# Performance work log

Measured on AMD Instinct MI355X. Metric: run time of the kernel, lower is better.

Reference implementation:

```python
import jax, jax.numpy as jnp
import numpy as np

TOP_K = 2
LORA_SCALE = 32.0 / 16.0  # alpha / rank


def setup_inputs() -> dict:
    key = jax.random.key(0)
    ks = jax.random.split(key, 11)
    N, D, F, E, R = 1024, 2048, 5632, 8, 16
    s = lambda k, shape, fan: jax.random.normal(k, shape, jnp.float32) / np.sqrt(fan)
    return {
        "x": jax.random.normal(ks[0], (N, D), jnp.float32),
        "gate_w": s(ks[1], (E, D), D),
        "W1": s(ks[2], (F, D), D),
        "W3": s(ks[3], (F, D), D),
        "W2": s(ks[4], (D, F), F),
        "A1": s(ks[5], (E, R, D), D),
        "B1": s(ks[6], (F, R), R)[None].repeat(E, 0) * 0.0 + s(ks[6], (E, F, R), R),
        "A3": s(ks[7], (E, R, D), D),
        "B3": s(ks[8], (E, F, R), R),
        "A2": s(ks[9], (E, R, F), F),
        "B2": s(ks[10], (E, D, R), R),
    }


def reference(x, gate_w, W1, W3, W2, A1, B1, A3, B3, A2, B2):
    # --- router: softmax over experts, top-k, renormalized combine weights ---
    logits = x @ gate_w.T                                   # [N, E]
    probs = jax.nn.softmax(logits, axis=-1)
    topw, topi = jax.lax.top_k(probs, TOP_K)                # [N, K]
    topw = topw / jnp.sum(topw, axis=-1, keepdims=True)
    E = gate_w.shape[0]
    w = jnp.sum(jax.nn.one_hot(topi, E, dtype=x.dtype) * topw[..., None], axis=1)  # [N, E]

    # --- experts: shared base weights + per-expert LoRA (fused SwiGLU) ---
    base1 = x @ W1.T                                        # [N, F]
    base3 = x @ W3.T                                        # [N, F]
    l1 = jnp.einsum("nd,erd->ner", x, A1)                   # rank-R bottleneck
    l3 = jnp.einsum("nd,erd->ner", x, A3)
    h1 = base1[:, None, :] + LORA_SCALE * jnp.einsum("ner,efr->nef", l1, B1)  # [N, E, F]
    h3 = base3[:, None, :] + LORA_SCALE * jnp.einsum("ner,efr->nef", l3, B3)
    s = jax.nn.silu(h1) * h3                                # [N, E, F]

    # down-projection: shared W2 applied to the routed mixture, plus per-expert LoRA
    s_mix = jnp.einsum("ne,nef->nf", w, s)                  # [N, F]
    out = s_mix @ W2.T                                      # [N, D]
    l2 = jnp.einsum("nef,erf->ner", s, A2) * (w[:, :, None] * LORA_SCALE)
    out = out + jnp.einsum("ner,edr->nd", l2, B2)           # [N, D]
    return out, logits
```

## Files before the change

kernel.cpp:

```cpp
#include <hip/hip_runtime.h>

typedef unsigned int u32;
typedef unsigned short u16;

#define N_TOK 1024
#define D_DIM 2048
#define F_DIM 5632
#define E_NUM 8
#define R_DIM 16
#define LSCALE 2.0f
#define FT 256
#define NT (F_DIM / FT)
#define TC 8
#define BN13 11520

typedef __bf16 bf16x8 __attribute__((ext_vector_type(8)));
typedef float f32x4 __attribute__((ext_vector_type(4)));
typedef u16 u16x8 __attribute__((ext_vector_type(8)));

__device__ inline u16 f2bf(float f) {
    u32 u = __builtin_bit_cast(u32, f);
    u32 r = (u + 0x7fffu + ((u >> 16) & 1u)) >> 16;
    return (u16)r;
}
__device__ inline float bf2f(u16 h) {
    u32 u = ((u32)h) << 16;
    return __builtin_bit_cast(float, u);
}

__global__ __launch_bounds__(256) void cvt_all(const float* __restrict__ x,
                                               const float* __restrict__ W1,
                                               const float* __restrict__ W3,
                                               const float* __restrict__ A1,
                                               const float* __restrict__ A3,
                                               const float* __restrict__ W2,
                                               const float* __restrict__ B1,
                                               const float* __restrict__ B3,
                                               u16* __restrict__ xb,
                                               u16* __restrict__ w13,
                                               u16* __restrict__ w2b,
                                               u16* __restrict__ b1b,
                                               u16* __restrict__ b3b) {
    int i = blockIdx.x * 256 + threadIdx.x;
    const float* src;
    u16* dst;
    int off;
    if (i < 524288)       { src = x;  dst = xb;             off = i; }
    else if (i < 3407872) { src = W1; dst = w13;            off = i - 524288; }
    else if (i < 6291456) { src = W3; dst = w13 + 11534336; off = i - 3407872; }
    else if (i < 6356992) { src = A1; dst = w13 + 23068672; off = i - 6291456; }
    else if (i < 6422528) { src = A3; dst = w13 + 23330816; off = i - 6356992; }
    else if (i < 9306112) { src = W2; dst = w2b;            off = i - 6422528; }
    else if (i < 9486336) { src = B1; dst = b1b;            off = i - 9306112; }
    else                  { src = B3; dst = b3b;            off = i - 9486336; }
    float4 v = ((const float4*)src)[off];
    union { u16 h[4]; ushort4 u4; } o;
    o.h[0] = f2bf(v.x); o.h[1] = f2bf(v.y); o.h[2] = f2bf(v.z); o.h[3] = f2bf(v.w);
    ((ushort4*)dst)[off] = o.u4;
}

__global__ __launch_bounds__(256) void a2_transpose(const float* __restrict__ A2,
                                                    u16* __restrict__ A2t) {
    int e = blockIdx.y;
    int f = blockIdx.x * 256 + threadIdx.x;
    u16 row[16];
#pragma unroll
    for (int r = 0; r < 16; ++r)
        row[r] = f2bf(A2[((size_t)e * R_DIM + r) * F_DIM + f]);
    u16* dst = A2t + ((size_t)e * F_DIM + f) * 16;
#pragma unroll
    for (int q = 0; q < 2; ++q)
        ((ulonglong2*)dst)[q] = ((ulonglong2*)row)[q];
}

__global__ __launch_bounds__(256) void router_kernel(const float* __restrict__ x,
                                                     const float* __restrict__ gw,
                                                     float* __restrict__ logits,
                                                     int* __restrict__ ridx,
                                                     float* __restrict__ rw) {
    int n = blockIdx.x;
    int tid = threadIdx.x;
    float part[E_NUM];
#pragma unroll
    for (int e = 0; e < E_NUM; ++e) part[e] = 0.f;
    const float* xr = x + (size_t)n * D_DIM;
    for (int d = tid; d < D_DIM; d += 256) {
        float xv = xr[d];
#pragma unroll
        for (int e = 0; e < E_NUM; ++e) part[e] += xv * gw[e * D_DIM + d];
    }
    __shared__ float sh[E_NUM][256];
#pragma unroll
    for (int e = 0; e < E_NUM; ++e) sh[e][tid] = part[e];
    __syncthreads();
    for (int off = 128; off > 0; off >>= 1) {
        if (tid < off) {
#pragma unroll
            for (int e = 0; e < E_NUM; ++e) sh[e][tid] += sh[e][tid + off];
        }
        __syncthreads();
    }
    if (tid == 0) {
        float lg[E_NUM], p[E_NUM];
        float mx = -1e30f;
        for (int e = 0; e < E_NUM; ++e) {
            lg[e] = sh[e][0];
            logits[n * E_NUM + e] = lg[e];
            if (lg[e] > mx) mx = lg[e];
        }
        float s = 0.f;
        for (int e = 0; e < E_NUM; ++e) { p[e] = expf(lg[e] - mx); s += p[e]; }
        for (int e = 0; e < E_NUM; ++e) p[e] /= s;
        int i1 = 0;
        for (int e = 1; e < E_NUM; ++e) if (p[e] > p[i1]) i1 = e;
        int i2 = (i1 == 0) ? 1 : 0;
        for (int e = 0; e < E_NUM; ++e) if (e != i1 && p[e] > p[i2]) i2 = e;
        float t = p[i1] + p[i2];
        ridx[n * 2] = i1; ridx[n * 2 + 1] = i2;
        rw[n * 2] = p[i1] / t; rw[n * 2 + 1] = p[i2] / t;
    }
}

__global__ __launch_bounds__(64) void zero_counts(int* counts) {
    if (threadIdx.x < E_NUM) counts[threadIdx.x] = 0;
}
__global__ __launch_bounds__(256) void build_lists(const int* __restrict__ ridx,
                                                   int* __restrict__ counts,
                                                   u32* __restrict__ lists) {
    int n = blockIdx.x * 256 + threadIdx.x;
    if (n >= N_TOK) return;
#pragma unroll
    for (int k = 0; k < 2; ++k) {
        int e = ridx[n * 2 + k];
        int slot = atomicAdd(&counts[e], 1);
        lists[e * N_TOK + slot] = (u32)n | ((u32)k << 16);
    }
}

__global__ __launch_bounds__(512, 2) void gemm256(const u16* __restrict__ A,
                                                  const u16* __restrict__ B,
                                                  float* __restrict__ C,
                                                  int N, int K, int kslice,
                                                  int mode, int ntm, int ntn) {
    __shared__ __align__(16) u16 sA[2][256 * 64];
    __shared__ __align__(16) u16 sB[2][256 * 64];

    const int nb = gridDim.x;
    const int f = blockIdx.x;
    const int q = nb >> 3, r = nb & 7;
    const int xcd = f & 7, lo = f >> 3;
    const int wg = (xcd < r ? xcd * (q + 1) : r * (q + 1) + (xcd - r) * q) + lo;

    const int mt = wg % ntm;
    const int t2 = wg / ntm;
    const int nt = t2 % ntn;
    const int zt = t2 / ntn;

    const int bm0 = mt * 256;
    const int bn0 = nt * 256;
    const int kb = zt * kslice;

    const int tid = threadIdx.x;
    const int lane = tid & 63;
    const int wave = tid >> 6;
    const int quad = lane >> 4;
    const int l16 = lane & 15;
    const int wm = (wave >> 2) * 128;
    const int wn = (wave & 3) * 64;

    f32x4 zero = {0.f, 0.f, 0.f, 0.f};
    f32x4 acc[8][4];
#pragma unroll
    for (int i = 0; i < 8; ++i)
#pragma unroll
        for (int j = 0; j < 4; ++j) acc[i][j] = zero;

    auto stage = [&](int buf, int k0) {
#pragma unroll
        for (int i = 0; i < 4; ++i) {
            int c = i * 512 + tid;
            int rr = c >> 3;
            int c8 = (c & 7) << 3;
            const u16* ga = A + (size_t)(bm0 + rr) * K + k0 + c8;
            const u16* gb = B + (size_t)(bn0 + rr) * K + k0 + c8;
            __builtin_amdgcn_global_load_lds((const __attribute__((address_space(1))) u32*)ga,
                                             (__attribute__((address_space(3))) u32*)(&sA[buf][c * 8]),
                                             16, 0, 0);
            __builtin_amdgcn_global_load_lds((const __attribute__((address_space(1))) u32*)gb,
                                             (__attribute__((address_space(3))) u32*)(&sB[buf][c * 8]),
                                             16, 0, 0);
        }
    };

    const int nk = kslice >> 6;
    int cur = 0;
    stage(0, kb);
    __syncthreads();

    for (int kt = 0; kt < nk; ++kt) {
        if (kt + 1 < nk) stage(cur ^ 1, kb + (kt + 1) * 64);
#pragma unroll
        for (int ks = 0; ks < 2; ++ks) {
            bf16x8 af[8], bfv[4];
#pragma unroll
            for (int mi = 0; mi < 8; ++mi)
                af[mi] = *(const bf16x8*)(&sA[cur][(wm + mi * 16 + l16) * 64 + ks * 32 + quad * 8]);
#pragma unroll
            for (int ni = 0; ni < 4; ++ni)
                bfv[ni] = *(const bf16x8*)(&sB[cur][(wn + ni * 16 + l16) * 64 + ks * 32 + quad * 8]);
#pragma unroll
            for (int mi = 0; mi < 8; ++mi)
#pragma unroll
                for (int ni = 0; ni < 4; ++ni)
                    acc[mi][ni] = __builtin_amdgcn_mfma_f32_16x16x32_bf16(af[mi], bfv[ni],
                                                                          acc[mi][ni], 0, 0, 0);
        }
        __syncthreads();
        cur ^= 1;
    }

#pragma unroll
    for (int mi = 0; mi < 8; ++mi)
#pragma unroll
        for (int ni = 0; ni < 4; ++ni) {
            int col = bn0 + wn + ni * 16 + l16;
#pragma unroll
            for (int i = 0; i < 4; ++i) {
                int row = bm0 + wm + mi * 16 + quad * 4 + i;
                if (mode == 1) {
                    ((u16*)C)[(size_t)row * N + col] = f2bf(acc[mi][ni][i]);
                } else if (mode == 2) {
                    unsafeAtomicAdd(&C[(size_t)row * N + col], acc[mi][ni][i]);
                } else {
                    C[(size_t)row * N + col] = acc[mi][ni][i];
                }
            }
        }
}

__global__ __launch_bounds__(256) void act_v2b(const u16* __restrict__ base13,
                                               const u16* __restrict__ B1b,
                                               const u16* __restrict__ B3b,
                                               const u32* __restrict__ lists,
                                               const int* __restrict__ counts,
                                               const float* __restrict__ rw,
                                               u16* __restrict__ sbuf) {
    const int ft = blockIdx.x;
    const int e  = blockIdx.y;
    const int z  = blockIdx.z;
    const int tid = threadIdx.x;
    const int lane = tid & 63;
    const int wave = tid >> 6;
    const int f_lane = ft * FT + lane * 4;

    u16x8 w1c[8], w3c[8];
    {
        const u16* p1 = B1b + ((size_t)e * F_DIM + f_lane) * 16;
        const u16* p3 = B3b + ((size_t)e * F_DIM + f_lane) * 16;
#pragma unroll
        for (int c = 0; c < 8; ++c) {
            w1c[c] = *(const u16x8*)(p1 + c * 8);
            w3c[c] = *(const u16x8*)(p3 + c * 8);
        }
    }

    const int T = counts[e];
    for (int i = z * 4 + wave; i < T; i += TC * 4) {
        u32 ent = lists[e * N_TOK + i];
        int n = (int)(ent & 0xFFFFu);
        int k = (int)(ent >> 16);
        float wt = rw[n * 2 + k];

        float la1[16], la3[16];
        {
            const u16x8* pl1 = (const u16x8*)(base13 + (size_t)n * BN13 + 11264 + e * 16);
            const u16x8* pl3 = (const u16x8*)(base13 + (size_t)n * BN13 + 11392 + e * 16);
#pragma unroll
            for (int h = 0; h < 2; ++h) {
                u16x8 t1 = pl1[h], t3 = pl3[h];
#pragma unroll
                for (int qq = 0; qq < 8; ++qq) {
                    la1[h * 8 + qq] = LSCALE * bf2f(t1[qq]);
                    la3[h * 8 + qq] = LSCALE * bf2f(t3[qq]);
                }
            }
        }

        ushort4 b1u = *(const ushort4*)(base13 + (size_t)n * BN13 + f_lane);
        ushort4 b3u = *(const ushort4*)(base13 + (size_t)n * BN13 + 5632 + f_lane);
        const u16* b1p = (const u16*)&b1u;
        const u16* b3p = (const u16*)&b3u;

        u16 sv[4];
#pragma unroll
        for (int j = 0; j < 4; ++j) {
            float h1 = bf2f(b1p[j]);
            float h3 = bf2f(b3p[j]);
#pragma unroll
            for (int qq = 0; qq < 8; ++qq) {
                h1 += la1[qq] * bf2f(w1c[2 * j][qq]);
                h3 += la3[qq] * bf2f(w3c[2 * j][qq]);
            }
#pragma unroll
            for (int qq = 0; qq < 8; ++qq) {
                h1 += la1[8 + qq] * bf2f(w1c[2 * j + 1][qq]);
                h3 += la3[8 + qq] * bf2f(w3c[2 * j + 1][qq]);
            }
            float sg = h1 / (1.f + __expf(-h1));
            sv[j] = f2bf(wt * sg * h3);
        }
        *(ushort4*)(sbuf + ((size_t)k * N_TOK + n) * F_DIM + f_lane) = *(ushort4*)sv;
    }
}

__global__ __launch_bounds__(256) void combine_kernel(const u16* __restrict__ sbuf,
                                                      u16* __restrict__ smix) {
    size_t i = ((size_t)blockIdx.x * 256 + threadIdx.x) * 8;
    u16x8 a = *(const u16x8*)(sbuf + i);
    u16x8 b = *(const u16x8*)(sbuf + (size_t)N_TOK * F_DIM + i);
    u16x8 o;
#pragma unroll
    for (int q = 0; q < 8; ++q) o[q] = f2bf(bf2f(a[q]) + bf2f(b[q]));
    *(u16x8*)(smix + i) = o;
}

__global__ __launch_bounds__(256) void lora_down_v3(const u16* __restrict__ sbuf,
                                                    const u16* __restrict__ A2t,
                                                    const int* __restrict__ ridx,
                                                    const float* __restrict__ B2,
                                                    float* __restrict__ out) {
    const int n = blockIdx.x, tid = threadIdx.x;
    __shared__ float part[2][32][16];
    __shared__ float fin[2][16];
    __shared__ int se[2];
    if (tid < 2) se[tid] = ridx[n * 2 + tid];
    __syncthreads();

    {
        const int k = tid >> 7;
        const int tt = tid & 127;
        const int rq = tt & 3;
        const int fc = tt >> 2;
        const int e = se[k];
        const u16* srow = sbuf + ((size_t)k * N_TOK + n) * F_DIM + fc * 176;
        const u16* arow = A2t + ((size_t)e * F_DIM + fc * 176) * 16 + rq * 4;
        float acc0 = 0.f, acc1 = 0.f, acc2 = 0.f, acc3 = 0.f;
#pragma unroll 4
        for (int f = 0; f < 176; ++f) {
            float sv = bf2f(srow[f]);
            ushort4 wr = *(const ushort4*)(arow + (size_t)f * 16);
            acc0 += sv * bf2f(wr.x);
            acc1 += sv * bf2f(wr.y);
            acc2 += sv * bf2f(wr.z);
            acc3 += sv * bf2f(wr.w);
        }
        part[k][fc][rq * 4 + 0] = acc0;
        part[k][fc][rq * 4 + 1] = acc1;
        part[k][fc][rq * 4 + 2] = acc2;
        part[k][fc][rq * 4 + 3] = acc3;
    }
    __syncthreads();
    if (tid < 32) {
        int k = tid >> 4, r = tid & 15;
        float s = 0.f;
#pragma unroll
        for (int fc = 0; fc < 32; ++fc) s += part[k][fc][r];
        fin[k][r] = LSCALE * s;
    }
    __syncthreads();

    float a0[16], a1v[16];
#pragma unroll
    for (int r = 0; r < 16; ++r) { a0[r] = fin[0][r]; a1v[r] = fin[1][r]; }
    const float* B2a = B2 + (size_t)se[0] * D_DIM * R_DIM;
    const float* B2b = B2 + (size_t)se[1] * D_DIM * R_DIM;
    float* orow = out + (size_t)n * D_DIM;
    for (int d = tid; d < D_DIM; d += 256) {
        const float4* pa = (const float4*)(B2a + (size_t)d * 16);
        const float4* pb = (const float4*)(B2b + (size_t)d * 16);
        float acc = 0.f;
#pragma unroll
        for (int q = 0; q < 4; ++q) {
            float4 va = pa[q];
            acc += a0[q * 4] * va.x + a0[q * 4 + 1] * va.y +
                   a0[q * 4 + 2] * va.z + a0[q * 4 + 3] * va.w;
            float4 vb = pb[q];
            acc += a1v[q * 4] * vb.x + a1v[q * 4 + 1] * vb.y +
                   a1v[q * 4 + 2] * vb.z + a1v[q * 4 + 3] * vb.w;
        }
        orow[d] = acc;
    }
}

extern "C" void kernel_launch(void* const* d_in, const int* in_sizes, int n_in,
                              void* d_out, int out_size, void* d_ws, size_t ws_size,
                              hipStream_t stream) {
    const float* x  = (const float*)d_in[0];
    const float* gw = (const float*)d_in[1];
    const float* W1 = (const float*)d_in[2];
    const float* W3 = (const float*)d_in[3];
    const float* W2 = (const float*)d_in[4];
    const float* A1 = (const float*)d_in[5];
    const float* B1 = (const float*)d_in[6];
    const float* A3 = (const float*)d_in[7];
    const float* B3 = (const float*)d_in[8];
    const float* A2 = (const float*)d_in[9];
    const float* B2 = (const float*)d_in[10];
    float* out = (float*)d_out;
    float* logits = out + (size_t)N_TOK * D_DIM;

    char* ws = (char*)d_ws;
    size_t off = 0;
    auto alloc = [&](size_t bytes) { char* p = ws + off; off += (bytes + 255) & ~(size_t)255; return p; };
    u16*   xb    = (u16*)alloc((size_t)N_TOK * D_DIM * 2);
    u16*   W13b  = (u16*)alloc((size_t)BN13 * D_DIM * 2);
    u16*   W2b   = (u16*)alloc((size_t)D_DIM * F_DIM * 2);
    u16*   base13= (u16*)alloc((size_t)N_TOK * BN13 * 2);
    int*   ridx  = (int*)alloc((size_t)N_TOK * 2 * 4);
    float* rwt   = (float*)alloc((size_t)N_TOK * 2 * 4);
    u16*   B1b   = (u16*)alloc((size_t)E_NUM * F_DIM * R_DIM * 2);
    u16*   B3b   = (u16*)alloc((size_t)E_NUM * F_DIM * R_DIM * 2);
    u16*   A2t   = (u16*)alloc((size_t)E_NUM * F_DIM * R_DIM * 2);
    int*   counts= (int*)alloc(64);
    u32*   lists = (u32*)alloc((size_t)E_NUM * N_TOK * 4);
    u16*   sbuf  = (u16*)alloc((size_t)2 * N_TOK * F_DIM * 2);
    u16*   smixb = (u16*)alloc((size_t)N_TOK * F_DIM * 2);
    (void)ws_size; (void)in_sizes; (void)n_in; (void)out_size;

    cvt_all<<<37760, 256, 0, stream>>>(x, W1, W3, A1, A3, W2, B1, B3,
                                       xb, W13b, W2b, B1b, B3b);
    a2_transpose<<<dim3(F_DIM / 256, E_NUM), 256, 0, stream>>>(A2, A2t);

    router_kernel<<<N_TOK, 256, 0, stream>>>(x, gw, logits, ridx, rwt);
    zero_counts<<<1, 64, 0, stream>>>(counts);
    build_lists<<<N_TOK / 256, 256, 0, stream>>>(ridx, counts, lists);

    gemm256<<<180, 512, 0, stream>>>(xb, W13b, (float*)base13,
                                     BN13, D_DIM, D_DIM, 1, 4, 45);

    act_v2b<<<dim3(NT, E_NUM, TC), 256, 0, stream>>>(base13, B1b, B3b,
                                                     lists, counts, rwt, sbuf);

    combine_kernel<<<(N_TOK * F_DIM / 8) / 256, 256, 0, stream>>>(sbuf, smixb);

    lora_down_v3<<<N_TOK, 256, 0, stream>>>(sbuf, A2t, ridx, B2, out);

    gemm256<<<256, 512, 0, stream>>>(smixb, W2b, out,
                                     D_DIM, F_DIM, 704, 2, 4, 8);
}
```

Measured before the change: 464.5 us.

## Restructure gemm256 mainloop into quadrant-staged pipeline with swizzled LDS

```diff
diff --git a/kernel.cpp b/kernel.cpp
--- a/kernel.cpp
+++ b/kernel.cpp
@@ -27,6 +27,11 @@
     u32 u = ((u32)h) << 16;
     return __builtin_bit_cast(float, u);
 }
+
+#define LGKM0() do { asm volatile("s_waitcnt lgkmcnt(0)" ::: "memory"); \
+                     __builtin_amdgcn_sched_barrier(0); } while (0)
+#define VMC(n)  do { asm volatile("s_waitcnt vmcnt(" #n ")" ::: "memory"); \
+                     __builtin_amdgcn_sched_barrier(0); } while (0)
 
 __global__ __launch_bounds__(256) void cvt_all(const float* __restrict__ x,
                                                const float* __restrict__ W1,
@@ -142,14 +147,13 @@
                                                   float* __restrict__ C,
                                                   int N, int K, int kslice,
                                                   int mode, int ntm, int ntn) {
-    __shared__ __align__(16) u16 sA[2][256 * 64];
-    __shared__ __align__(16) u16 sB[2][256 * 64];
+    __shared__ __align__(16) u16 lds[2][2][2][256 * 32];
 
     const int nb = gridDim.x;
-    const int f = blockIdx.x;
-    const int q = nb >> 3, r = nb & 7;
-    const int xcd = f & 7, lo = f >> 3;
-    const int wg = (xcd < r ? xcd * (q + 1) : r * (q + 1) + (xcd - r) * q) + lo;
+    const int fb = blockIdx.x;
+    const int qq = nb >> 3, rr = nb & 7;
+    const int xcd = fb & 7, lo = fb >> 3;
+    const int wg = (xcd < rr ? xcd * (qq + 1) : rr * (qq + 1) + (xcd - rr) * qq) + lo;
 
     const int mt = wg % ntm;
     const int t2 = wg / ntm;
@@ -165,6 +169,7 @@
     const int wave = tid >> 6;
     const int quad = lane >> 4;
     const int l16 = lane & 15;
+    const int swz = (l16 & 8) << 1;
     const int wm = (wave >> 2) * 128;
     const int wn = (wave & 3) * 64;
 
@@ -175,48 +180,139 @@
 #pragma unroll
         for (int j = 0; j < 4; ++j) acc[i][j] = zero;
 
-    auto stage = [&](int buf, int k0) {
-#pragma unroll
-        for (int i = 0; i < 4; ++i) {
-            int c = i * 512 + tid;
-            int rr = c >> 3;
-            int c8 = (c & 7) << 3;
-            const u16* ga = A + (size_t)(bm0 + rr) * K + k0 + c8;
-            const u16* gb = B + (size_t)(bn0 + rr) * K + k0 + c8;
-            __builtin_amdgcn_global_load_lds((const __attribute__((address_space(1))) u32*)ga,
-                                             (__attribute__((address_space(3))) u32*)(&sA[buf][c * 8]),
+    auto stageHalf = [&](const u16* __restrict__ G, int mat, int buf, int h,
+                         int k0, int rowBase) {
+#pragma unroll
+        for (int j = 0; j < 2; ++j) {
+            int seg = wave * 2 + j;
+            int plane = seg >> 3;
+            int rb = seg & 7;
+            int r = h * 128 + rb * 16 + (lane >> 2);
+            int slot = lane & 3;
+            int gcol = k0 + plane * 32 + ((slot * 8) ^ ((r & 8) << 1));
+            const u16* gp = G + (size_t)(rowBase + r) * K + gcol;
+            u16* lp = &lds[mat][buf][plane][(h * 128 + rb * 16) * 32] + lane * 8;
+            __builtin_amdgcn_global_load_lds((const __attribute__((address_space(1))) u32*)gp,
+                                             (__attribute__((address_space(3))) u32*)lp,
                                              16, 0, 0);
-            __builtin_amdgcn_global_load_lds((const __attribute__((address_space(1))) u32*)gb,
-                                             (__attribute__((address_space(3))) u32*)(&sB[buf][c * 8]),
-                                             16, 0, 0);
         }
     };
 
     const int nk = kslice >> 6;
-    int cur = 0;
-    stage(0, kb);
-    __syncthreads();
-
-    for (int kt = 0; kt < nk; ++kt) {
-        if (kt + 1 < nk) stage(cur ^ 1, kb + (kt + 1) * 64);
-#pragma unroll
-        for (int ks = 0; ks < 2; ++ks) {
-            bf16x8 af[8], bfv[4];
-#pragma unroll
-            for (int mi = 0; mi < 8; ++mi)
-                af[mi] = *(const bf16x8*)(&sA[cur][(wm + mi * 16 + l16) * 64 + ks * 32 + quad * 8]);
-#pragma unroll
-            for (int ni = 0; ni < 4; ++ni)
-                bfv[ni] = *(const bf16x8*)(&sB[cur][(wn + ni * 16 + l16) * 64 + ks * 32 + quad * 8]);
-#pragma unroll
-            for (int mi = 0; mi < 8; ++mi)
-#pragma unroll
-                for (int ni = 0; ni < 4; ++ni)
-                    acc[mi][ni] = __builtin_amdgcn_mfma_f32_16x16x32_bf16(af[mi], bfv[ni],
-                                                                          acc[mi][ni], 0, 0, 0);
-        }
-        __syncthreads();
-        cur ^= 1;
+
+    stageHalf(A, 0, 0, 0, kb, bm0);
+    stageHalf(A, 0, 0, 1, kb, bm0);
+    stageHalf(B, 1, 0, 0, kb, bn0);
+    stageHalf(B, 1, 0, 1, kb, bn0);
+    stageHalf(A, 0, 1, 0, kb + 64, bm0);
+    stageHalf(A, 0, 1, 1, kb + 64, bm0);
+    VMC(4);
+    __builtin_amdgcn_s_barrier();
+
+    bf16x8 af[8][2];
+    for (int t = 0; t < nk; ++t) {
+        const int buf = t & 1;
+        const int k0 = kb + t * 64;
+
+        {
+            bf16x8 bf[2][2];
+#pragma unroll
+            for (int mi = 0; mi < 4; ++mi)
+#pragma unroll
+                for (int ks = 0; ks < 2; ++ks)
+                    af[mi][ks] = *(const bf16x8*)&lds[0][buf][ks]
+                        [(wm + mi * 16 + l16) * 32 + ((quad * 8) ^ swz)];
+#pragma unroll
+            for (int ni = 0; ni < 2; ++ni)
+#pragma unroll
+                for (int ks = 0; ks < 2; ++ks)
+                    bf[ni][ks] = *(const bf16x8*)&lds[1][buf][ks]
+                        [(wn + ni * 16 + l16) * 32 + ((quad * 8) ^ swz)];
+            if (t + 1 < nk) stageHalf(B, 1, buf ^ 1, 0, k0 + 64, bn0);
+            __builtin_amdgcn_s_barrier();
+            LGKM0();
+            __builtin_amdgcn_s_setprio(1);
+#pragma unroll
+            for (int mi = 0; mi < 4; ++mi)
+#pragma unroll
+                for (int ni = 0; ni < 2; ++ni)
+#pragma unroll
+                    for (int ks = 0; ks < 2; ++ks)
+                        acc[mi][ni] = __builtin_amdgcn_mfma_f32_16x16x32_bf16(
+                            af[mi][ks], bf[ni][ks], acc[mi][ni], 0, 0, 0);
+            __builtin_amdgcn_s_setprio(0);
+            __builtin_amdgcn_s_barrier();
+        }
+
+        {
+            bf16x8 bf[2][2];
+#pragma unroll
+            for (int mi = 0; mi < 4; ++mi)
+#pragma unroll
+                for (int ks = 0; ks < 2; ++ks)
+                    af[4 + mi][ks] = *(const bf16x8*)&lds[0][buf][ks]
+                        [(wm + (4 + mi) * 16 + l16) * 32 + ((quad * 8) ^ swz)];
+#pragma unroll
+            for (int ni = 0; ni < 2; ++ni)
+#pragma unroll
+                for (int ks = 0; ks < 2; ++ks)
+                    bf[ni][ks] = *(const bf16x8*)&lds[1][buf][ks]
+                        [(wn + (2 + ni) * 16 + l16) * 32 + ((quad * 8) ^ swz)];
+            if (t + 1 < nk) stageHalf(B, 1, buf ^ 1, 1, k0 + 64, bn0);
+            __builtin_amdgcn_s_barrier();
+            LGKM0();
+            __builtin_amdgcn_s_setprio(1);
+#pragma unroll
+            for (int mi = 0; mi < 4; ++mi)
+#pragma unroll
+                for (int ni = 0; ni < 2; ++ni)
+#pragma unroll
+                    for (int ks = 0; ks < 2; ++ks)
+                        acc[mi][2 + ni] = __builtin_amdgcn_mfma_f32_16x16x32_bf16(
+                            af[mi][ks], bf[ni][ks], acc[mi][2 + ni], 0, 0, 0);
+            __builtin_amdgcn_s_setprio(0);
+            __builtin_amdgcn_s_barrier();
+
+            if (t + 2 < nk) stageHalf(A, 0, buf, 0, k0 + 128, bm0);
+            __builtin_amdgcn_s_barrier();
+            __builtin_amdgcn_s_setprio(1);
+#pragma unroll
+            for (int mi = 0; mi < 4; ++mi)
+#pragma unroll
+                for (int ni = 0; ni < 2; ++ni)
+#pragma unroll
+                    for (int ks = 0; ks < 2; ++ks)
+                        acc[4 + mi][2 + ni] = __builtin_amdgcn_mfma_f32_16x16x32_bf16(
+                            af[4 + mi][ks], bf[ni][ks], acc[4 + mi][2 + ni], 0, 0, 0);
+            __builtin_amdgcn_s_setprio(0);
+            __builtin_amdgcn_s_barrier();
+        }
+
+        {
+            bf16x8 bf[2][2];
+#pragma unroll
+            for (int ni = 0; ni < 2; ++ni)
+#pragma unroll
+                for (int ks = 0; ks < 2; ++ks)
+                    bf[ni][ks] = *(const bf16x8*)&lds[1][buf][ks]
+                        [(wn + ni * 16 + l16) * 32 + ((quad * 8) ^ swz)];
+            if (t + 2 < nk) stageHalf(A, 0, buf, 1, k0 + 128, bm0);
+            __builtin_amdgcn_s_barrier();
+            LGKM0();
+            __builtin_amdgcn_s_setprio(1);
+#pragma unroll
+            for (int mi = 0; mi < 4; ++mi)
+#pragma unroll
+                for (int ni = 0; ni < 2; ++ni)
+#pragma unroll
+                    for (int ks = 0; ks < 2; ++ks)
+                        acc[4 + mi][ni] = __builtin_amdgcn_mfma_f32_16x16x32_bf16(
+                            af[4 + mi][ks], bf[ni][ks], acc[4 + mi][ni], 0, 0, 0);
+            __builtin_amdgcn_s_setprio(0);
+            if (t < nk - 2)       { VMC(4); }
+            else if (t == nk - 2) { VMC(0); }
+            __builtin_amdgcn_s_barrier();
+        }
     }
 
 #pragma unroll
```

After: 440.0 us. 1.06x faster.
